# Kernel tuning notes

Measured on AMD Instinct MI355X. Metric: run time of the kernel, lower is better.

Reference implementation:

```python
import jax, jax.numpy as jnp
import numpy as np

K = 32          # num_sets (experts)
D_IN = 10       # input_size
D_H = 20        # hidden_size
D_OUT = 1       # output_size
B = 262144      # batch


def setup_inputs() -> dict:
    key = jax.random.key(0)
    ks = jax.random.split(key, 6)
    # Kaiming-uniform-ish init scale like torch Linear defaults
    s1 = 1.0 / np.sqrt(D_IN)
    s2 = 1.0 / np.sqrt(D_H)
    return {
        "input_data": jax.random.normal(ks[0], (B, D_IN), dtype=jnp.float32),
        "W1": jax.random.uniform(ks[1], (K, D_H, D_IN), jnp.float32, -s1, s1),
        "b1": jax.random.uniform(ks[2], (K, D_H), jnp.float32, -s1, s1),
        "W2": jax.random.uniform(ks[3], (K, D_OUT, D_H), jnp.float32, -s2, s2),
        "b2": jax.random.uniform(ks[4], (K, D_OUT), jnp.float32, -s2, s2),
        "prototypes": jax.random.normal(ks[5], (K, D_IN), dtype=jnp.float32),
    }


def reference(input_data, W1, b1, W2, b2, prototypes):
    # All K tiny experts as one batched GEMM: [B,K,H]
    h = jax.nn.relu(jnp.einsum("bi,khi->bkh", input_data, W1) + b1[None])
    preds = jnp.einsum("bkh,koh->bko", h, W2) + b2[None]          # [B,K,O]
    # Distance-based softmax gating over experts
    diff = input_data[:, None, :] - prototypes[None, :, :]        # [B,K,D]
    dist = jnp.sqrt(jnp.sum(diff * diff, axis=2))                 # [B,K]
    attn = jax.nn.softmax(-dist, axis=1)                          # [B,K]
    return jnp.sum(preds * attn[:, :, None], axis=1)              # [B,O]
```

## Files before the change

kernel.cpp:

```cpp
#include <hip/hip_runtime.h>


#define KX 32
#define DIN 10
#define DH 20
#define BLOCK 512
#define WPB 8
#define TPW 2

typedef short bf16x8 __attribute__((ext_vector_type(8)));
typedef float f32x16 __attribute__((ext_vector_type(16)));
typedef float v2f    __attribute__((ext_vector_type(2)));

#define ZERO16 {0.f,0.f,0.f,0.f, 0.f,0.f,0.f,0.f, 0.f,0.f,0.f,0.f, 0.f,0.f,0.f,0.f}

__device__ inline unsigned short f2bf(float f) {
    unsigned int u = __float_as_uint(f);
    unsigned int r = u + 0x7fffu + ((u >> 16) & 1u);
    return (unsigned short)(r >> 16);
}

union BFU { bf16x8 v; unsigned short s[8]; };

__global__ __launch_bounds__(BLOCK, 4) void moe_kernel(
    const float* __restrict__ x,
    const float* __restrict__ W1,
    const float* __restrict__ b1,
    const float* __restrict__ W2,
    const float* __restrict__ b2,
    const float* __restrict__ proto,
    float* __restrict__ out,
    int B)
{
    __shared__ bf16x8 s_af2[DH * 64];
    __shared__ __attribute__((aligned(16))) float s_w2c[DH * 32];
    __shared__ bf16x8 s_pf[64];
    __shared__ float2 s_gk[32];

    const int tid = threadIdx.x;

    for (int idx = tid; idx < DH * 64; idx += BLOCK) {
        const int jj = idx >> 6, rem = idx & 63;
        const int e = rem >> 1, ks = rem & 1;
        BFU u;
#pragma unroll
        for (int j = 0; j < 8; ++j) {
            const int kk = ks * 8 + j;
            float v = 0.f;
            if (kk < DIN) v = W1[(e * DH + jj) * DIN + kk];
            else if (kk == DIN) v = b1[e * DH + jj];
            u.s[j] = f2bf(v);
        }
        s_af2[idx] = u.v;
    }
    for (int idx = tid; idx < DH * 32; idx += BLOCK) {
        const int jj = idx >> 5, rem = idx & 31;
        const int hf = rem >> 4, q = rem & 15;
        const int p = (q & 3) + 8 * (q >> 2) + 4 * hf;
        s_w2c[idx] = W2[p * DH + jj];
    }
    if (tid < 64) {
        const int m = tid & 31, kb = (tid >> 5) * 8;
        BFU u;
#pragma unroll
        for (int j = 0; j < 8; ++j) {
            const int kk = kb + j;
            u.s[j] = f2bf(kk < DIN ? proto[m * DIN + kk] : 0.f);
        }
        s_pf[tid] = u.v;
    }
    if (tid < 32) {
        const int hf = tid >> 4, q = tid & 15;
        const int p = (q & 3) + 8 * (q >> 2) + 4 * hf;
        float s = 0.f;
#pragma unroll
        for (int i = 0; i < DIN; ++i) { const float v = proto[p * DIN + i]; s = fmaf(v, v, s); }
        s_gk[tid] = make_float2(s, b2[p]);
    }
    __syncthreads();

    const int lane = tid & 63;
    const int wave = tid >> 6;
    const int half = lane >> 5;
    const int col  = lane & 31;
    const bf16x8 pfrag = s_pf[lane];
    const f32x16 kZero = ZERO16;
    const int aoff = (col << 1) + half;

    int    row[TPW];
    bf16x8 xfrag[TPW];
    float  xn2[TPW];
    v2f    pa[TPW][8];

#pragma unroll
    for (int t = 0; t < TPW; ++t) {
        row[t] = ((blockIdx.x * WPB + wave) * TPW + t) * 32 + col;
        const int rr = (row[t] < B) ? row[t] : (B - 1);

        float xe[8];
        const float* xr = x + (size_t)rr * DIN;
        if (half == 0) {
#pragma unroll
            for (int i = 0; i < 4; ++i) {
                const float2 v = *(const float2*)(xr + 2 * i);
                xe[2 * i] = v.x; xe[2 * i + 1] = v.y;
            }
        } else {
            const float2 v = *(const float2*)(xr + 8);
            xe[0] = v.x; xe[1] = v.y; xe[2] = 1.f;
            xe[3] = 0.f; xe[4] = 0.f; xe[5] = 0.f; xe[6] = 0.f; xe[7] = 0.f;
        }
        BFU xu;
#pragma unroll
        for (int j = 0; j < 8; ++j) xu.s[j] = f2bf(xe[j]);
        xfrag[t] = xu.v;

        float part;
        if (half == 0) {
            part = 0.f;
#pragma unroll
            for (int j = 0; j < 8; ++j) part = fmaf(xe[j], xe[j], part);
        } else {
            part = fmaf(xe[0], xe[0], xe[1] * xe[1]);
        }
        xn2[t] = part + __shfl_xor(part, 32);

#pragma unroll
        for (int i = 0; i < 8; ++i) pa[t][i] = v2f{0.f, 0.f};
    }

    const float4* w2base = (const float4*)s_w2c + (half << 2);
#pragma unroll 2
    for (int jj = 0; jj < DH; ++jj) {
        const bf16x8 a = s_af2[(jj << 6) + aoff];
        const float4* w4 = w2base + (jj << 3);
        const float4 w0 = w4[0], w1v = w4[1], w2v = w4[2], w3v = w4[3];

#pragma unroll
        for (int t = 0; t < TPW; ++t) {
            const f32x16 c = __builtin_amdgcn_mfma_f32_32x32x16_bf16(a, xfrag[t], kZero, 0, 0, 0);
            v2f r;
            r = __builtin_elementwise_max(v2f{c[0],  c[1]},  v2f{0.f, 0.f});
            pa[t][0] = __builtin_elementwise_fma(r, v2f{w0.x,  w0.y},  pa[t][0]);
            r = __builtin_elementwise_max(v2f{c[2],  c[3]},  v2f{0.f, 0.f});
            pa[t][1] = __builtin_elementwise_fma(r, v2f{w0.z,  w0.w},  pa[t][1]);
            r = __builtin_elementwise_max(v2f{c[4],  c[5]},  v2f{0.f, 0.f});
            pa[t][2] = __builtin_elementwise_fma(r, v2f{w1v.x, w1v.y}, pa[t][2]);
            r = __builtin_elementwise_max(v2f{c[6],  c[7]},  v2f{0.f, 0.f});
            pa[t][3] = __builtin_elementwise_fma(r, v2f{w1v.z, w1v.w}, pa[t][3]);
            r = __builtin_elementwise_max(v2f{c[8],  c[9]},  v2f{0.f, 0.f});
            pa[t][4] = __builtin_elementwise_fma(r, v2f{w2v.x, w2v.y}, pa[t][4]);
            r = __builtin_elementwise_max(v2f{c[10], c[11]}, v2f{0.f, 0.f});
            pa[t][5] = __builtin_elementwise_fma(r, v2f{w2v.z, w2v.w}, pa[t][5]);
            r = __builtin_elementwise_max(v2f{c[12], c[13]}, v2f{0.f, 0.f});
            pa[t][6] = __builtin_elementwise_fma(r, v2f{w3v.x, w3v.y}, pa[t][6]);
            r = __builtin_elementwise_max(v2f{c[14], c[15]}, v2f{0.f, 0.f});
            pa[t][7] = __builtin_elementwise_fma(r, v2f{w3v.z, w3v.w}, pa[t][7]);
        }
    }

    const float2* gkh = s_gk + half * 16;
#pragma unroll
    for (int t = 0; t < TPW; ++t) {
        const f32x16 dg = __builtin_amdgcn_mfma_f32_32x32x16_bf16(pfrag, xfrag[t], kZero, 0, 0, 0);
        float ds = 0.f, ns = 0.f;
#pragma unroll
        for (int q = 0; q < 16; ++q) {
            const float2 gk = gkh[q];
            float d2 = fmaf(dg[q], -2.f, xn2[t] + gk.x);
            d2 = fmaxf(d2, 0.f);
            const float g = __expf(-__fsqrt_rn(d2));
            ds += g;
            const v2f pp = pa[t][q >> 1];
            const float pq = (q & 1) ? pp.y : pp.x;
            ns = fmaf(g, pq + gk.y, ns);
        }
        const float nst = ns + __shfl_xor(ns, 32);
        const float dst = ds + __shfl_xor(ds, 32);
        if (half == 0 && row[t] < B) out[row[t]] = nst / dst;
    }
}

extern "C" void kernel_launch(void* const* d_in, const int* in_sizes, int n_in,
                              void* d_out, int out_size, void* d_ws, size_t ws_size,
                              hipStream_t stream) {
    const float* x     = (const float*)d_in[0];
    const float* W1    = (const float*)d_in[1];
    const float* b1    = (const float*)d_in[2];
    const float* W2    = (const float*)d_in[3];
    const float* b2    = (const float*)d_in[4];
    const float* proto = (const float*)d_in[5];
    float* out = (float*)d_out;

    const int B = out_size;
    const int rows_per_block = WPB * TPW * 32;
    const int grid = (B + rows_per_block - 1) / rows_per_block;
    hipLaunchKernelGGL(moe_kernel, dim3(grid), dim3(BLOCK), 0, stream,
                       x, W1, b1, W2, b2, proto, out, B);
}
```

Measured before the change: 89.45 us.

## Fold log2e into distance terms, preload b2 into accumulators, double block size

```diff
diff --git a/kernel.cpp b/kernel.cpp
--- a/kernel.cpp
+++ b/kernel.cpp
@@ -4,9 +4,12 @@
 #define KX 32
 #define DIN 10
 #define DH 20
-#define BLOCK 512
-#define WPB 8
+#define BLOCK 1024
+#define WPB 16
 #define TPW 2
+
+#define LOG2E_SQ 2.0813689810056077f
+#define NEG2_LOG2E_SQ -4.1627379620112154f
 
 typedef short bf16x8 __attribute__((ext_vector_type(8)));
 typedef float f32x16 __attribute__((ext_vector_type(16)));
@@ -35,7 +38,8 @@
     __shared__ bf16x8 s_af2[DH * 64];
     __shared__ __attribute__((aligned(16))) float s_w2c[DH * 32];
     __shared__ bf16x8 s_pf[64];
-    __shared__ float2 s_gk[32];
+    __shared__ float  s_gk[32];
+    __shared__ float2 s_b2p[16];
 
     const int tid = threadIdx.x;
 
@@ -75,7 +79,14 @@
         float s = 0.f;
 #pragma unroll
         for (int i = 0; i < DIN; ++i) { const float v = proto[p * DIN + i]; s = fmaf(v, v, s); }
-        s_gk[tid] = make_float2(s, b2[p]);
+        s_gk[tid] = s * LOG2E_SQ;
+    }
+    if (tid < 16) {
+        const int hf = tid >> 3, i = tid & 7;
+        const int q0 = 2 * i, q1 = 2 * i + 1;
+        const int p0 = (q0 & 3) + 8 * (q0 >> 2) + 4 * hf;
+        const int p1 = (q1 & 3) + 8 * (q1 >> 2) + 4 * hf;
+        s_b2p[tid] = make_float2(b2[p0], b2[p1]);
     }
     __syncthreads();
 
@@ -123,10 +134,13 @@
         } else {
             part = fmaf(xe[0], xe[0], xe[1] * xe[1]);
         }
-        xn2[t] = part + __shfl_xor(part, 32);
-
-#pragma unroll
-        for (int i = 0; i < 8; ++i) pa[t][i] = v2f{0.f, 0.f};
+        xn2[t] = (part + __shfl_xor(part, 32)) * LOG2E_SQ;
+
+#pragma unroll
+        for (int i = 0; i < 8; ++i) {
+            const float2 bp = s_b2p[half * 8 + i];
+            pa[t][i] = v2f{bp.x, bp.y};
+        }
     }
 
     const float4* w2base = (const float4*)s_w2c + (half << 2);
@@ -159,25 +173,24 @@
         }
     }
 
-    const float2* gkh = s_gk + half * 16;
+    const float* gkx = s_gk + half * 16;
 #pragma unroll
     for (int t = 0; t < TPW; ++t) {
         const f32x16 dg = __builtin_amdgcn_mfma_f32_32x32x16_bf16(pfrag, xfrag[t], kZero, 0, 0, 0);
         float ds = 0.f, ns = 0.f;
 #pragma unroll
         for (int q = 0; q < 16; ++q) {
-            const float2 gk = gkh[q];
-            float d2 = fmaf(dg[q], -2.f, xn2[t] + gk.x);
+            float d2 = fmaf(dg[q], NEG2_LOG2E_SQ, xn2[t] + gkx[q]);
             d2 = fmaxf(d2, 0.f);
-            const float g = __expf(-__fsqrt_rn(d2));
+            const float g = __builtin_amdgcn_exp2f(-__fsqrt_rn(d2));
             ds += g;
             const v2f pp = pa[t][q >> 1];
             const float pq = (q & 1) ? pp.y : pp.x;
-            ns = fmaf(g, pq + gk.y, ns);
+            ns = fmaf(g, pq, ns);
         }
         const float nst = ns + __shfl_xor(ns, 32);
         const float dst = ds + __shfl_xor(ds, 32);
-        if (half == 0 && row[t] < B) out[row[t]] = nst / dst;
+        if (half == 0 && row[t] < B) out[row[t]] = nst * __builtin_amdgcn_rcpf(dst);
     }
 }
 
```

Result: no change. 88.86 us (-0.7%).
